# Kernel optimization log

Hardware: AMD Instinct MI355X
Metric: run time of the kernel (lower is better)

Reference implementation:

```python
import jax, jax.numpy as jnp
import numpy as np

N_NODES = 16384
N_EDGES = 196608
N_ELEM = 8
C = 32              # hidden channels per l-block
LMAX = 3
SH_DIM = 16         # (LMAX+1)^2
NUM_BESSEL = 8
R_MAX = 5.0
P_CUT = 5.0
H_RAD = 64
AVG_NEIGH = 12.0
N_LAYERS = 2
L_SLICES = ((0, 1), (1, 4), (4, 9), (9, 16))  # l = 0..3 blocks


def real_sph_harm(u):
    # u: [E,3] unit vectors -> real spherical harmonics up to l=3, component-normalized. [E,16]
    x, y, z = u[:, 0], u[:, 1], u[:, 2]
    x2, y2, z2 = x * x, y * y, z * z
    sh = [
        jnp.ones_like(x),
        jnp.sqrt(3.) * x, jnp.sqrt(3.) * y, jnp.sqrt(3.) * z,
        jnp.sqrt(15.) * x * y, jnp.sqrt(15.) * y * z,
        jnp.sqrt(5.) / 2. * (3. * z2 - 1.), jnp.sqrt(15.) * x * z,
        jnp.sqrt(15.) / 2. * (x2 - y2),
        jnp.sqrt(35. / 8.) * y * (3. * x2 - y2), jnp.sqrt(105.) * x * y * z,
        jnp.sqrt(21. / 8.) * y * (5. * z2 - 1.), jnp.sqrt(7.) / 2. * z * (5. * z2 - 3.),
        jnp.sqrt(21. / 8.) * x * (5. * z2 - 1.), jnp.sqrt(105.) / 2. * z * (x2 - y2),
        jnp.sqrt(35. / 8.) * x * (x2 - 3. * y2),
    ]
    return jnp.stack(sh, axis=-1)


def bessel_cutoff(r):
    # Bessel radial basis * polynomial cutoff (MACE radial embedding). r: [E] -> [E, NUM_BESSEL]
    u = r / R_MAX
    n = jnp.arange(1, NUM_BESSEL + 1, dtype=r.dtype)
    safe_r = jnp.maximum(r, 1e-9)
    rb = jnp.sqrt(2.0 / R_MAX) * jnp.sin(jnp.pi * n * u[:, None]) / safe_r[:, None]
    p = P_CUT
    fc = 1.0 - (p + 1.) * (p + 2.) / 2. * u ** p + p * (p + 2.) * u ** (p + 1.) - p * (p + 1.) / 2. * u ** (p + 2.)
    fc = fc * (u < 1.0).astype(r.dtype)
    return rb * fc[:, None]


def per_l_linear(a, W):
    # equivariant per-l channel mixing. a: [N,C,16], W: [4,C,C]
    outs = [jnp.einsum('nci,co->noi', a[:, :, s:e], W[l]) for l, (s, e) in enumerate(L_SLICES)]
    return jnp.concatenate(outs, axis=-1)


def mace_descriptors(atom_pos, node_attrs, shifts, edge_index,
                     W_embed, W1, W2, W3, W4, Wlin, Wskip, w2, w3, Wprod):
    snd, rcv = edge_index[0], edge_index[1]
    vec = atom_pos[rcv] - atom_pos[snd] + shifts            # [E,3]
    length = jnp.sqrt(jnp.sum(vec * vec, axis=-1) + 1e-18)  # [E]
    unit = vec / length[:, None]
    edge_attrs = real_sph_harm(unit)                        # [E,16]
    edge_feats = bessel_cutoff(length)                      # [E,8]

    node_scal = node_attrs @ W_embed                        # [N,C] node embedding (l=0)
    node_feats = jnp.zeros((atom_pos.shape[0], C, SH_DIM), dtype=atom_pos.dtype).at[:, :, 0].set(node_scal)

    descs = []
    for i in range(N_LAYERS):
        # radial MLP -> per-edge tensor-product weights
        h = jax.nn.silu(edge_feats @ W1[i])
        h = jax.nn.silu(h @ W2[i])
        h = jax.nn.silu(h @ W3[i])
        tpw = (h @ W4[i]).reshape(-1, C, SH_DIM)            # [E,C,16]
        # gather -> channelwise tensor product with edge spherical harmonics
        s = node_feats[:, :, 0][snd]                        # [E,C] invariant sender feats
        msg = tpw * edge_attrs[:, None, :] * s[:, :, None]  # [E,C,16]
        # scatter-add aggregation
        agg = jax.ops.segment_sum(msg.reshape(-1, C * SH_DIM), rcv,
                                  num_segments=N_NODES) / AVG_NEIGH
        a = per_l_linear(agg.reshape(-1, C, SH_DIM), Wlin[i])
        # element-dependent residual (skip tensor product with one-hot node attrs)
        sc = jnp.einsum('nz,ncm,zco->nom', node_attrs, node_feats, Wskip[i])
        # symmetric-contraction-style product block (correlation up to 3, invariants)
        inv = a[:, :, 0]
        p2 = jnp.sum(a * a, axis=-1)                        # power-spectrum invariant [N,C]
        b0 = inv + w2[i] * p2 + w3[i] * inv * p2
        b = a.at[:, :, 0].set(b0)
        node_feats = per_l_linear(b, Wprod[i]) + sc
        descs.append(node_feats[:, :, 0])                   # invariant slice
    return jnp.concatenate(descs, axis=-1)                  # [N, N_LAYERS*C]


def setup_inputs() -> dict:
    key = jax.random.key(0)
    ks = jax.random.split(key, 16)
    atom_pos = jax.random.normal(ks[0], (N_NODES, 3), dtype=jnp.float32) * 1.8
    elem = jax.random.randint(ks[1], (N_NODES,), 0, N_ELEM)
    node_attrs = jax.nn.one_hot(elem, N_ELEM, dtype=jnp.float32)
    shifts = jnp.zeros((N_EDGES, 3), dtype=jnp.float32)
    edge_index = jax.random.randint(ks[2], (2, N_EDGES), 0, N_NODES)
    f32 = jnp.float32
    W_embed = jax.random.normal(ks[3], (N_ELEM, C), f32) / np.sqrt(N_ELEM)
    W1 = jax.random.normal(ks[4], (N_LAYERS, NUM_BESSEL, H_RAD), f32) / np.sqrt(NUM_BESSEL)
    W2 = jax.random.normal(ks[5], (N_LAYERS, H_RAD, H_RAD), f32) / np.sqrt(H_RAD)
    W3 = jax.random.normal(ks[6], (N_LAYERS, H_RAD, H_RAD), f32) / np.sqrt(H_RAD)
    W4 = jax.random.normal(ks[7], (N_LAYERS, H_RAD, C * SH_DIM), f32) / np.sqrt(H_RAD)
    Wlin = jax.random.normal(ks[8], (N_LAYERS, 4, C, C), f32) / np.sqrt(C)
    Wskip = jax.random.normal(ks[9], (N_LAYERS, N_ELEM, C, C), f32) / np.sqrt(N_ELEM * C)
    w2 = jax.random.normal(ks[10], (N_LAYERS, C), f32) * 0.1
    w3 = jax.random.normal(ks[11], (N_LAYERS, C), f32) * 0.1
    Wprod = jax.random.normal(ks[12], (N_LAYERS, 4, C, C), f32) / np.sqrt(C)
    return {"atom_pos": atom_pos, "node_attrs": node_attrs, "shifts": shifts,
            "edge_index": edge_index, "W_embed": W_embed, "W1": W1, "W2": W2,
            "W3": W3, "W4": W4, "Wlin": Wlin, "Wskip": Wskip, "w2": w2,
            "w3": w3, "Wprod": Wprod}


def reference(atom_pos, node_attrs, shifts, edge_index, W_embed, W1, W2, W3, W4,
              Wlin, Wskip, w2, w3, Wprod):
    return mace_descriptors(atom_pos, node_attrs, shifts, edge_index,
                            W_embed, W1, W2, W3, W4, Wlin, Wskip, w2, w3, Wprod)
```

## Files before the change

### kernel.cpp

```cpp
#include <hip/hip_runtime.h>
#include <math.h>

#define N_NODES_C 16384
#define N_EDGES_C 196608
#define MAX_TILES 32768

typedef short bf16x8 __attribute__((ext_vector_type(8)));
typedef float f32x4 __attribute__((ext_vector_type(4)));
typedef float f32x8 __attribute__((ext_vector_type(8)));

__device__ __forceinline__ float silu_f(float x) {
  return x * __builtin_amdgcn_rcpf(1.0f + __expf(-x));
}

__global__ void k_count(const int* __restrict__ rcv, int* __restrict__ counts) {
  int e = blockIdx.x * 256 + threadIdx.x;
  atomicAdd(&counts[rcv[e]], 1);
}

__global__ __launch_bounds__(1024) void k_scan(const int* __restrict__ counts,
                                               int* __restrict__ row_start,
                                               int* __restrict__ cursor,
                                               int* __restrict__ tstart) {
  __shared__ int s1a[1024];
  __shared__ int s2a[1024];
  const int tid = threadIdx.x;
  int loc[16];
  int s1 = 0, s2 = 0;
#pragma unroll
  for (int i = 0; i < 16; ++i) {
    loc[i] = counts[tid * 16 + i];
    s1 += loc[i];
    s2 += (loc[i] + 15) >> 4;
  }
  s1a[tid] = s1;
  s2a[tid] = s2;
  __syncthreads();
  for (int off = 1; off < 1024; off <<= 1) {
    int t1 = (tid >= off) ? s1a[tid - off] : 0;
    int t2 = (tid >= off) ? s2a[tid - off] : 0;
    __syncthreads();
    s1a[tid] += t1;
    s2a[tid] += t2;
    __syncthreads();
  }
  int e1 = s1a[tid] - s1, e2 = s2a[tid] - s2;
#pragma unroll
  for (int i = 0; i < 16; ++i) {
    row_start[tid * 16 + i] = e1;
    cursor[tid * 16 + i] = e1;
    tstart[tid * 16 + i] = e2;
    e1 += loc[i];
    e2 += (loc[i] + 15) >> 4;
  }
  if (tid == 1023) {
    row_start[N_NODES_C] = e1;
    tstart[N_NODES_C] = e2;
  }
}

__global__ void k_fill(const int* __restrict__ rcv, int* __restrict__ cursor,
                       int* __restrict__ elist) {
  int e = blockIdx.x * 256 + threadIdx.x;
  int slot = atomicAdd(&cursor[rcv[e]], 1);
  elist[slot] = e;
}

__global__ void k_tiles(const int* __restrict__ row_start, const int* __restrict__ tstart,
                        int2* __restrict__ tdesc) {
  const int n = blockIdx.x * 256 + threadIdx.x;
  const int e0 = row_start[n], e1 = row_start[n + 1];
  const int cnt = e1 - e0;
  const int nt = (cnt + 15) >> 4;
  const int t0 = tstart[n];
  const unsigned mbit = (nt > 1) ? 0x80000000u : 0u;
  for (int j = 0; j < nt; ++j) {
    int len = cnt - 16 * j;
    if (len > 16) len = 16;
    tdesc[t0 + j] = make_int2((int)((unsigned)n | ((unsigned)len << 20) | mbit), e0 + 16 * j);
  }
}

__global__ void k_elem(const float* __restrict__ attrs, int* __restrict__ elem) {
  int n = blockIdx.x * 256 + threadIdx.x;
  const float* a = attrs + n * 8;
  int best = 0;
  float bv = a[0];
#pragma unroll
  for (int z = 1; z < 8; ++z) {
    if (a[z] > bv) { bv = a[z]; best = z; }
  }
  elem[n] = best;
}

__global__ void k_embed(const float* __restrict__ attrs, const float* __restrict__ Wemb,
                        float* __restrict__ scal0, float* __restrict__ nf) {
  int gid = blockIdx.x * 256 + threadIdx.x;
  int n = gid >> 5, c = gid & 31;
  float s = 0.f;
#pragma unroll
  for (int z = 0; z < 8; ++z) s = fmaf(attrs[n * 8 + z], Wemb[z * 32 + c], s);
  scal0[gid] = s;
  float* row = nf + (size_t)n * 512 + c * 16;
  *(float4*)&row[0] = make_float4(s, 0.f, 0.f, 0.f);
  *(float4*)&row[4] = make_float4(0.f, 0.f, 0.f, 0.f);
  *(float4*)&row[8] = make_float4(0.f, 0.f, 0.f, 0.f);
  *(float4*)&row[12] = make_float4(0.f, 0.f, 0.f, 0.f);
}

__global__ __launch_bounds__(256, 3) void k_radial(
    const float* __restrict__ pos, const float* __restrict__ shifts,
    const int* __restrict__ snd, const int* __restrict__ rcv,
    const int* __restrict__ elist, const float* __restrict__ scal,
    const float* __restrict__ W1g, const float* __restrict__ W2g,
    const float* __restrict__ W3g, unsigned short* __restrict__ h3,
    float* __restrict__ sedge, float* __restrict__ Yout, const int writeY) {
  __shared__ __align__(16) float efs[4][32][8];
  __shared__ __align__(16) float hbs[4][2][64];
  const int wid = threadIdx.x >> 6, lane = threadIdx.x & 63;
  float w1c[8], w2c[64], w3c[64];
#pragma unroll
  for (int k = 0; k < 8; ++k) w1c[k] = W1g[k * 64 + lane];
#pragma unroll
  for (int k = 0; k < 64; ++k) w2c[k] = W2g[k * 64 + lane];
#pragma unroll
  for (int k = 0; k < 64; ++k) w3c[k] = W3g[k * 64 + lane];

  const int base = (blockIdx.x * 4 + wid) * 32;

  if (lane < 32) {
    const int p = base + lane;
    const int e = elist[p];
    const int sn = snd[e], rc = rcv[e];
    const float vx = pos[rc * 3 + 0] - pos[sn * 3 + 0] + shifts[e * 3 + 0];
    const float vy = pos[rc * 3 + 1] - pos[sn * 3 + 1] + shifts[e * 3 + 1];
    const float vz = pos[rc * 3 + 2] - pos[sn * 3 + 2] + shifts[e * 3 + 2];
    const float len = __builtin_amdgcn_sqrtf(vx * vx + vy * vy + vz * vz + 1e-18f);
    const float u = len * 0.2f;
    float fc = 0.f;
    if (u < 1.0f) {
      const float u2 = u * u, u5 = u2 * u2 * u;
      fc = 1.0f - 21.0f * u5 + 35.0f * u5 * u - 15.0f * u5 * u2;
    }
    const float pref = 0.6324555320336759f * fc * __builtin_amdgcn_rcpf(fmaxf(len, 1e-9f));
    float efv[8];
#pragma unroll
    for (int k = 0; k < 8; ++k) {
      const float pin = 3.14159274f * (float)(k + 1);
      efv[k] = pref * __sinf(pin * u);
    }
    *(float4*)&efs[wid][lane][0] = make_float4(efv[0], efv[1], efv[2], efv[3]);
    *(float4*)&efs[wid][lane][4] = make_float4(efv[4], efv[5], efv[6], efv[7]);

    if (writeY) {
      const float il = __builtin_amdgcn_rcpf(len);
      const float x = vx * il, y = vy * il, z = vz * il;
      const float x2 = x * x, y2 = y * y, z2 = z * z;
      const float s3 = 1.7320508075688772f;
      const float s15 = 3.872983346207417f;
      const float s5h = 1.118033988749895f;
      const float s35_8 = 2.091650066335189f;
      const float s105 = 10.246950765959598f;
      const float s21_8 = 1.6201851746019651f;
      const float s7h = 1.3228756555322954f;
      const float s105h = 5.123475382979799f;
      float* yp = Yout + (size_t)p * 16;
      *(float4*)&yp[0] = make_float4(1.f, s3 * x, s3 * y, s3 * z);
      *(float4*)&yp[4] = make_float4(s15 * x * y, s15 * y * z, s5h * (3.f * z2 - 1.f), s15 * x * z);
      *(float4*)&yp[8] = make_float4(0.5f * s15 * (x2 - y2), s35_8 * y * (3.f * x2 - y2),
                                     s105 * x * y * z, s21_8 * y * (5.f * z2 - 1.f));
      *(float4*)&yp[12] = make_float4(s7h * z * (5.f * z2 - 3.f), s21_8 * x * (5.f * z2 - 1.f),
                                      s105h * z * (x2 - y2), s35_8 * x * (x2 - 3.f * y2));
    }
  }

  {
    const int p2 = base + (lane >> 1);
    const int e2 = elist[p2];
    const int sn2 = snd[e2];
    const int co = (lane & 1) * 16;
    const float* sp = scal + (size_t)sn2 * 32 + co;
    float* dp = sedge + (size_t)p2 * 32 + co;
    *(float4*)&dp[0] = *(const float4*)&sp[0];
    *(float4*)&dp[4] = *(const float4*)&sp[4];
    *(float4*)&dp[8] = *(const float4*)&sp[8];
    *(float4*)&dp[12] = *(const float4*)&sp[12];
  }

  for (int t = 0; t < 16; ++t) {
    const float4 eA0 = *(const float4*)&efs[wid][t][0];
    const float4 eA1 = *(const float4*)&efs[wid][t][4];
    const float4 eB0 = *(const float4*)&efs[wid][t + 16][0];
    const float4 eB1 = *(const float4*)&efs[wid][t + 16][4];
    float aA = eA0.x * w1c[0], aB = eB0.x * w1c[0];
    aA = fmaf(eA0.y, w1c[1], aA); aB = fmaf(eB0.y, w1c[1], aB);
    aA = fmaf(eA0.z, w1c[2], aA); aB = fmaf(eB0.z, w1c[2], aB);
    aA = fmaf(eA0.w, w1c[3], aA); aB = fmaf(eB0.w, w1c[3], aB);
    aA = fmaf(eA1.x, w1c[4], aA); aB = fmaf(eB1.x, w1c[4], aB);
    aA = fmaf(eA1.y, w1c[5], aA); aB = fmaf(eB1.y, w1c[5], aB);
    aA = fmaf(eA1.z, w1c[6], aA); aB = fmaf(eB1.z, w1c[6], aB);
    aA = fmaf(eA1.w, w1c[7], aA); aB = fmaf(eB1.w, w1c[7], aB);
    hbs[wid][0][lane] = silu_f(aA);
    hbs[wid][1][lane] = silu_f(aB);
    float pA0 = 0.f, pA1 = 0.f, pA2 = 0.f, pA3 = 0.f;
    float pB0 = 0.f, pB1 = 0.f, pB2 = 0.f, pB3 = 0.f;
#pragma unroll
    for (int k4 = 0; k4 < 16; ++k4) {
      const float4 hA = *(const float4*)&hbs[wid][0][k4 * 4];
      const float4 hB = *(const float4*)&hbs[wid][1][k4 * 4];
      pA0 = fmaf(hA.x, w2c[k4 * 4 + 0], pA0); pB0 = fmaf(hB.x, w2c[k4 * 4 + 0], pB0);
      pA1 = fmaf(hA.y, w2c[k4 * 4 + 1], pA1); pB1 = fmaf(hB.y, w2c[k4 * 4 + 1], pB1);
      pA2 = fmaf(hA.z, w2c[k4 * 4 + 2], pA2); pB2 = fmaf(hB.z, w2c[k4 * 4 + 2], pB2);
      pA3 = fmaf(hA.w, w2c[k4 * 4 + 3], pA3); pB3 = fmaf(hB.w, w2c[k4 * 4 + 3], pB3);
    }
    hbs[wid][0][lane] = silu_f((pA0 + pA1) + (pA2 + pA3));
    hbs[wid][1][lane] = silu_f((pB0 + pB1) + (pB2 + pB3));
    pA0 = pA1 = pA2 = pA3 = 0.f;
    pB0 = pB1 = pB2 = pB3 = 0.f;
#pragma unroll
    for (int k4 = 0; k4 < 16; ++k4) {
      const float4 hA = *(const float4*)&hbs[wid][0][k4 * 4];
      const float4 hB = *(const float4*)&hbs[wid][1][k4 * 4];
      pA0 = fmaf(hA.x, w3c[k4 * 4 + 0], pA0); pB0 = fmaf(hB.x, w3c[k4 * 4 + 0], pB0);
      pA1 = fmaf(hA.y, w3c[k4 * 4 + 1], pA1); pB1 = fmaf(hB.y, w3c[k4 * 4 + 1], pB1);
      pA2 = fmaf(hA.z, w3c[k4 * 4 + 2], pA2); pB2 = fmaf(hB.z, w3c[k4 * 4 + 2], pB2);
      pA3 = fmaf(hA.w, w3c[k4 * 4 + 3], pA3); pB3 = fmaf(hB.w, w3c[k4 * 4 + 3], pB3);
    }
    const float hvA = silu_f((pA0 + pA1) + (pA2 + pA3));
    const float hvB = silu_f((pB0 + pB1) + (pB2 + pB3));
    const unsigned hbA = __float_as_uint(hvA) & 0xFFFF0000u;
    const unsigned hbB = __float_as_uint(hvB) & 0xFFFF0000u;
    const float loA = hvA - __uint_as_float(hbA);
    const float loB = hvB - __uint_as_float(hbB);
    h3[(size_t)(base + t) * 128 + lane] = (unsigned short)(hbA >> 16);
    h3[(size_t)(base + t) * 128 + 64 + lane] = (unsigned short)(__float_as_uint(loA) >> 16);
    h3[(size_t)(base + 16 + t) * 128 + lane] = (unsigned short)(hbB >> 16);
    h3[(size_t)(base + 16 + t) * 128 + 64 + lane] = (unsigned short)(__float_as_uint(loB) >> 16);
  }
}

#define TLOAD(AX, YX, SX, MX, PX, tix)                                        \
  {                                                                           \
    const int tic = ((tix) < ntiles) ? (tix) : (ntiles - 1);                  \
    const int2 td = tdesc[tic];                                               \
    MX = (unsigned)td.x;                                                      \
    PX = td.y;                                                                \
    const unsigned short* hp = h3 + (size_t)(PX + lm) * 128 + grp * 8;        \
    AX##0 = *(const bf16x8*)(hp);                                             \
    AX##1 = *(const bf16x8*)(hp + 32);                                        \
    AX##2 = *(const bf16x8*)(hp + 64);                                        \
    AX##3 = *(const bf16x8*)(hp + 96);                                        \
    _Pragma("unroll") for (int r = 0; r < 4; ++r) {                           \
      const int pr = PX + grp * 4 + r;                                        \
      YX[r] = Yb[(size_t)pr * 16 + lm];                                       \
      SX[r] = *(const float4*)&sedge[(size_t)pr * 32 + cg * 4];               \
    }                                                                         \
  }

#define TCOMP(AX, YX, SX, MX, PX, tix)                                        \
  {                                                                           \
    const int node = (int)(MX & 0x3FFFu);                                     \
    const int len = (int)((MX >> 20) & 31u);                                  \
    const bool multi = (MX & 0x80000000u) != 0u;                              \
    float ys[4][4];                                                           \
    _Pragma("unroll") for (int r = 0; r < 4; ++r) {                           \
      const int rr = grp * 4 + r;                                             \
      const float Yv = (rr < len) ? YX[r] * inv12 : 0.f;                      \
      ys[r][0] = Yv * SX[r].x;                                                \
      ys[r][1] = Yv * SX[r].y;                                                \
      ys[r][2] = Yv * SX[r].z;                                                \
      ys[r][3] = Yv * SX[r].w;                                                \
    }                                                                         \
    float outv[4];                                                            \
    _Pragma("unroll") for (int t = 0; t < 4; ++t) {                           \
      f32x4 acc = {0.f, 0.f, 0.f, 0.f};                                       \
      acc = __builtin_amdgcn_mfma_f32_16x16x32_bf16(AX##0, bhi[t][0], acc, 0, 0, 0); \
      acc = __builtin_amdgcn_mfma_f32_16x16x32_bf16(AX##1, bhi[t][1], acc, 0, 0, 0); \
      acc = __builtin_amdgcn_mfma_f32_16x16x32_bf16(AX##2, bhi[t][0], acc, 0, 0, 0); \
      acc = __builtin_amdgcn_mfma_f32_16x16x32_bf16(AX##3, bhi[t][1], acc, 0, 0, 0); \
      acc = __builtin_amdgcn_mfma_f32_16x16x32_bf16(AX##0, blo[t][0], acc, 0, 0, 0); \
      acc = __builtin_amdgcn_mfma_f32_16x16x32_bf16(AX##1, blo[t][1], acc, 0, 0, 0); \
      float cp = acc[0] * ys[0][t];                                           \
      cp = fmaf(acc[1], ys[1][t], cp);                                        \
      cp = fmaf(acc[2], ys[2][t], cp);                                        \
      cp = fmaf(acc[3], ys[3][t], cp);                                        \
      cp += __shfl_xor(cp, 16);                                               \
      cp += __shfl_xor(cp, 32);                                               \
      outv[t] = cp;                                                           \
    }                                                                         \
    float sel = outv[0];                                                      \
    sel = (grp == 1) ? outv[1] : sel;                                         \
    sel = (grp == 2) ? outv[2] : sel;                                         \
    sel = (grp == 3) ? outv[3] : sel;                                         \
    if ((tix) < ntiles) {                                                     \
      float* ap = &agg[(size_t)node * 512 + cg * 64 + grp * 16 + lm];         \
      if (multi)                                                              \
        atomicAdd(ap, sel);                                                   \
      else                                                                    \
        *ap = sel;                                                            \
    }                                                                         \
  }

__global__ __launch_bounds__(256, 2) void k_gather(
    const unsigned short* __restrict__ h3, const float* __restrict__ W4g,
    const float* __restrict__ Yb, const float* __restrict__ sedge,
    const int2* __restrict__ tdesc, const int* __restrict__ ntiles_ptr,
    float* __restrict__ agg) {
  const int bid = blockIdx.x;
  const int xcd = bid & 7, q = bid >> 3, half = q & 1;
  const int s = ((q >> 1) << 3) | xcd;
  const int w = threadIdx.x >> 6, lane = threadIdx.x & 63;
  const int grp = lane >> 4, lm = lane & 15;
  const int cg = half * 4 + w;
  const float inv12 = 1.0f / 12.0f;

  bf16x8 bhi[4][2], blo[4][2];
#pragma unroll
  for (int t = 0; t < 4; ++t) {
    const int col = cg * 64 + t * 16 + lm;
#pragma unroll
    for (int kk = 0; kk < 2; ++kk) {
#pragma unroll
      for (int j = 0; j < 8; ++j) {
        const float wv = W4g[(kk * 32 + grp * 8 + j) * 512 + col];
        const unsigned hb = __float_as_uint(wv) & 0xFFFF0000u;
        bhi[t][kk][j] = (short)(hb >> 16);
        blo[t][kk][j] = (short)(__float_as_uint(wv - __uint_as_float(hb)) >> 16);
      }
    }
  }

  const int ntiles = *ntiles_ptr;
  const int chunk = (ntiles + 1023) >> 10;
  const int tbeg = s * chunk;

  bf16x8 aA0, aA1, aA2, aA3, aB0, aB1, aB2, aB3;
  float yA[4], yB[4];
  float4 sA[4], sB[4];
  unsigned mA, mB;
  int pA, pB;

  TLOAD(aA, yA, sA, mA, pA, tbeg);
  int j = 0;
  while (true) {
    TLOAD(aB, yB, sB, mB, pB, tbeg + j + 1);
    TCOMP(aA, yA, sA, mA, pA, tbeg + j);
    ++j;
    if (j >= chunk) break;
    TLOAD(aA, yA, sA, mA, pA, tbeg + j + 1);
    TCOMP(aB, yB, sB, mB, pB, tbeg + j);
    ++j;
    if (j >= chunk) break;
  }
}

__global__ __launch_bounds__(256) void k_node(
    const float* __restrict__ agg, float* __restrict__ nf,
    const float* __restrict__ Wlin, const float* __restrict__ Wprod,
    const float* __restrict__ Wskip, const float* __restrict__ w2v,
    const float* __restrict__ w3v, const int* __restrict__ elem,
    float* __restrict__ scal_out, float* __restrict__ dout, const int layer) {
  __shared__ __align__(16) float aggs[8][512];
  __shared__ __align__(16) float nfs[8][512];
  __shared__ float bs[8][544];
  const int tid = threadIdx.x;
  const int n0 = blockIdx.x * 8;
  for (int i = tid; i < 1024; i += 256) {
    const int nl = i >> 7, qq = i & 127;
    ((f32x4*)aggs)[i] = ((const f32x4*)agg)[(size_t)(n0 + nl) * 128 + qq];
    ((f32x4*)nfs)[i] = ((const f32x4*)nf)[(size_t)(n0 + nl) * 128 + qq];
  }
  __syncthreads();
  const int nl = tid >> 5, o = tid & 31;
  const int n = n0 + nl;
  constexpr int SLa[4] = {0, 1, 4, 9};
  constexpr int ELa[4] = {1, 4, 9, 16};
  float a[16];
#pragma unroll
  for (int m = 0; m < 16; ++m) a[m] = 0.f;
#pragma unroll
  for (int l = 0; l < 4; ++l) {
    for (int c = 0; c < 32; ++c) {
      const float w = Wlin[(l * 32 + c) * 32 + o];
#pragma unroll
      for (int m = SLa[l]; m < ELa[l]; ++m) a[m] = fmaf(aggs[nl][c * 16 + m], w, a[m]);
    }
  }
  const float inv = a[0];
  float p2 = 0.f;
#pragma unroll
  for (int m = 0; m < 16; ++m) p2 = fmaf(a[m], a[m], p2);
  a[0] = inv + w2v[o] * p2 + w3v[o] * inv * p2;
#pragma unroll
  for (int m = 0; m < 16; ++m) bs[nl][o * 17 + m] = a[m];
  __syncthreads();
  float outv[16];
#pragma unroll
  for (int m = 0; m < 16; ++m) outv[m] = 0.f;
#pragma unroll
  for (int l = 0; l < 4; ++l) {
    for (int c = 0; c < 32; ++c) {
      const float w = Wprod[(l * 32 + c) * 32 + o];
#pragma unroll
      for (int m = SLa[l]; m < ELa[l]; ++m) outv[m] = fmaf(bs[nl][c * 17 + m], w, outv[m]);
    }
  }
  const int z = elem[n];
  const float* wsk = Wskip + z * 1024;
  for (int c = 0; c < 32; ++c) {
    const float w = wsk[c * 32 + o];
#pragma unroll
    for (int m = 0; m < 16; ++m) outv[m] = fmaf(nfs[nl][c * 16 + m], w, outv[m]);
  }
  float* op = nf + (size_t)n * 512 + o * 16;
  *(float4*)&op[0] = make_float4(outv[0], outv[1], outv[2], outv[3]);
  *(float4*)&op[4] = make_float4(outv[4], outv[5], outv[6], outv[7]);
  *(float4*)&op[8] = make_float4(outv[8], outv[9], outv[10], outv[11]);
  *(float4*)&op[12] = make_float4(outv[12], outv[13], outv[14], outv[15]);
  scal_out[n * 32 + o] = outv[0];
  dout[(size_t)n * 64 + layer * 32 + o] = outv[0];
}

extern "C" void kernel_launch(void* const* d_in, const int* in_sizes, int n_in,
                              void* d_out, int out_size, void* d_ws, size_t ws_size,
                              hipStream_t stream) {
  const float* pos = (const float*)d_in[0];
  const float* attrs = (const float*)d_in[1];
  const float* shifts = (const float*)d_in[2];
  const int* eidx = (const int*)d_in[3];
  const float* W_embed = (const float*)d_in[4];
  const float* W1 = (const float*)d_in[5];
  const float* W2 = (const float*)d_in[6];
  const float* W3 = (const float*)d_in[7];
  const float* W4 = (const float*)d_in[8];
  const float* Wlin = (const float*)d_in[9];
  const float* Wskip = (const float*)d_in[10];
  const float* w2v = (const float*)d_in[11];
  const float* w3v = (const float*)d_in[12];
  const float* Wprod = (const float*)d_in[13];
  float* out = (float*)d_out;
  const int* snd = eidx;
  const int* rcv = eidx + N_EDGES_C;

  char* p = (char*)d_ws;
  auto take = [&](size_t bytes) {
    char* q = p;
    p += (bytes + 255) & ~(size_t)255;
    return q;
  };
  int* counts = (int*)take((size_t)N_NODES_C * 4);
  int* row_start = (int*)take((size_t)(N_NODES_C + 1) * 4);
  int* cursor = (int*)take((size_t)N_NODES_C * 4);
  int* tstart = (int*)take((size_t)(N_NODES_C + 1) * 4);
  int* elist = (int*)take((size_t)N_EDGES_C * 4);
  int2* tdesc = (int2*)take((size_t)MAX_TILES * 8);
  int* elem = (int*)take((size_t)N_NODES_C * 4);
  float* Ybuf = (float*)take((size_t)(N_EDGES_C + 16) * 16 * 4);
  unsigned short* h3 = (unsigned short*)take((size_t)(N_EDGES_C + 16) * 128 * 2);
  float* sedge = (float*)take((size_t)(N_EDGES_C + 16) * 32 * 4);
  float* agg = (float*)take((size_t)N_NODES_C * 512 * 4);
  float* nf = (float*)take((size_t)N_NODES_C * 512 * 4);
  float* scal0 = (float*)take((size_t)N_NODES_C * 32 * 4);
  float* scal1 = (float*)take((size_t)N_NODES_C * 32 * 4);
  (void)ws_size; (void)in_sizes; (void)n_in; (void)out_size;

  hipMemsetAsync(counts, 0, (size_t)N_NODES_C * 4, stream);
  k_count<<<N_EDGES_C / 256, 256, 0, stream>>>(rcv, counts);
  k_scan<<<1, 1024, 0, stream>>>(counts, row_start, cursor, tstart);
  k_fill<<<N_EDGES_C / 256, 256, 0, stream>>>(rcv, cursor, elist);
  k_tiles<<<N_NODES_C / 256, 256, 0, stream>>>(row_start, tstart, tdesc);
  k_elem<<<N_NODES_C / 256, 256, 0, stream>>>(attrs, elem);
  k_embed<<<N_NODES_C * 32 / 256, 256, 0, stream>>>(attrs, W_embed, scal0, nf);

  for (int i = 0; i < 2; ++i) {
    k_radial<<<1536, 256, 0, stream>>>(pos, shifts, snd, rcv, elist,
                                       i == 0 ? scal0 : scal1,
                                       W1 + (size_t)i * 8 * 64, W2 + (size_t)i * 64 * 64,
                                       W3 + (size_t)i * 64 * 64, h3, sedge, Ybuf,
                                       i == 0 ? 1 : 0);
    hipMemsetAsync(agg, 0, (size_t)N_NODES_C * 512 * 4, stream);
    k_gather<<<2048, 256, 0, stream>>>(h3, W4 + (size_t)i * 64 * 512, Ybuf, sedge,
                                       tdesc, tstart + N_NODES_C, agg);
    k_node<<<N_NODES_C / 8, 256, 0, stream>>>(agg, nf, Wlin + (size_t)i * 4096,
                                              Wprod + (size_t)i * 4096,
                                              Wskip + (size_t)i * 8192,
                                              w2v + (size_t)i * 32, w3v + (size_t)i * 32,
                                              elem, scal1, out, i);
  }
}
```

Measured before the change: 518.6 us.

## Deepen gather kernel prefetch to a four-slot ring and halve the grid

Replaces the two-stage double buffer in the edge-gather kernel with a four-slot ring. Tile descriptors are fetched four tiles ahead, and h3, Y and sedge data two tiles ahead, with the Y·sedge scaling done at load time. The grid drops from 2048 to 1024 blocks, so each block handles a chunk twice as long, rounded up to a multiple of four. The aim is to hide global-load latency behind the MFMA work. In exchange, register pressure rises, and the padded chunks add extra clamped tail iterations.

```diff
diff --git a/kernel.cpp b/kernel.cpp
--- a/kernel.cpp
+++ b/kernel.cpp
@@ -239,51 +239,56 @@
   }
 }
 
-#define TLOAD(AX, YX, SX, MX, PX, tix)                                        \
+#define MLOAD(K, tix)                                                         \
   {                                                                           \
     const int tic = ((tix) < ntiles) ? (tix) : (ntiles - 1);                  \
     const int2 td = tdesc[tic];                                               \
-    MX = (unsigned)td.x;                                                      \
-    PX = td.y;                                                                \
-    const unsigned short* hp = h3 + (size_t)(PX + lm) * 128 + grp * 8;        \
-    AX##0 = *(const bf16x8*)(hp);                                             \
-    AX##1 = *(const bf16x8*)(hp + 32);                                        \
-    AX##2 = *(const bf16x8*)(hp + 64);                                        \
-    AX##3 = *(const bf16x8*)(hp + 96);                                        \
-    _Pragma("unroll") for (int r = 0; r < 4; ++r) {                           \
-      const int pr = PX + grp * 4 + r;                                        \
-      YX[r] = Yb[(size_t)pr * 16 + lm];                                       \
-      SX[r] = *(const float4*)&sedge[(size_t)pr * 32 + cg * 4];               \
-    }                                                                         \
-  }
-
-#define TCOMP(AX, YX, SX, MX, PX, tix)                                        \
+    M[K] = (unsigned)td.x;                                                    \
+    P[K] = td.y;                                                              \
+  }
+
+#define DLOAD(K2)                                                             \
   {                                                                           \
-    const int node = (int)(MX & 0x3FFFu);                                     \
-    const int len = (int)((MX >> 20) & 31u);                                  \
-    const bool multi = (MX & 0x80000000u) != 0u;                              \
-    float ys[4][4];                                                           \
+    const int p0 = P[K2];                                                     \
+    const int lend = (int)((M[K2] >> 20) & 31u);                              \
+    const unsigned short* hp = h3 + (size_t)(p0 + lm) * 128 + grp * 8;        \
+    A[K2][0] = *(const bf16x8*)(hp);                                          \
+    A[K2][1] = *(const bf16x8*)(hp + 32);                                     \
+    A[K2][2] = *(const bf16x8*)(hp + 64);                                     \
+    A[K2][3] = *(const bf16x8*)(hp + 96);                                     \
     _Pragma("unroll") for (int r = 0; r < 4; ++r) {                           \
       const int rr = grp * 4 + r;                                             \
-      const float Yv = (rr < len) ? YX[r] * inv12 : 0.f;                      \
-      ys[r][0] = Yv * SX[r].x;                                                \
-      ys[r][1] = Yv * SX[r].y;                                                \
-      ys[r][2] = Yv * SX[r].z;                                                \
-      ys[r][3] = Yv * SX[r].w;                                                \
+      const int pr = p0 + rr;                                                 \
+      const float yr = Yb[(size_t)pr * 16 + lm];                              \
+      const float Yv = ((rr < lend) ? yr : 0.f) * inv12;                      \
+      const float4 s4 = *(const float4*)&sedge[(size_t)pr * 32 + cg * 4];     \
+      YS[K2][r][0] = Yv * s4.x;                                               \
+      YS[K2][r][1] = Yv * s4.y;                                               \
+      YS[K2][r][2] = Yv * s4.z;                                               \
+      YS[K2][r][3] = Yv * s4.w;                                               \
     }                                                                         \
+  }
+
+#define STEP(K)                                                               \
+  {                                                                           \
+    const unsigned mcur = M[K];                                               \
+    MLOAD(K, tb + 4);                                                         \
+    DLOAD((K + 2) & 3);                                                       \
+    const int node = (int)(mcur & 0x3FFFu);                                   \
+    const bool multi = (mcur & 0x80000000u) != 0u;                            \
     float outv[4];                                                            \
     _Pragma("unroll") for (int t = 0; t < 4; ++t) {                           \
       f32x4 acc = {0.f, 0.f, 0.f, 0.f};                                       \
-      acc = __builtin_amdgcn_mfma_f32_16x16x32_bf16(AX##0, bhi[t][0], acc, 0, 0, 0); \
-      acc = __builtin_amdgcn_mfma_f32_16x16x32_bf16(AX##1, bhi[t][1], acc, 0, 0, 0); \
-      acc = __builtin_amdgcn_mfma_f32_16x16x32_bf16(AX##2, bhi[t][0], acc, 0, 0, 0); \
-      acc = __builtin_amdgcn_mfma_f32_16x16x32_bf16(AX##3, bhi[t][1], acc, 0, 0, 0); \
-      acc = __builtin_amdgcn_mfma_f32_16x16x32_bf16(AX##0, blo[t][0], acc, 0, 0, 0); \
-      acc = __builtin_amdgcn_mfma_f32_16x16x32_bf16(AX##1, blo[t][1], acc, 0, 0, 0); \
-      float cp = acc[0] * ys[0][t];                                           \
-      cp = fmaf(acc[1], ys[1][t], cp);                                        \
-      cp = fmaf(acc[2], ys[2][t], cp);                                        \
-      cp = fmaf(acc[3], ys[3][t], cp);                                        \
+      acc = __builtin_amdgcn_mfma_f32_16x16x32_bf16(A[K][0], bhi[t][0], acc, 0, 0, 0); \
+      acc = __builtin_amdgcn_mfma_f32_16x16x32_bf16(A[K][1], bhi[t][1], acc, 0, 0, 0); \
+      acc = __builtin_amdgcn_mfma_f32_16x16x32_bf16(A[K][2], bhi[t][0], acc, 0, 0, 0); \
+      acc = __builtin_amdgcn_mfma_f32_16x16x32_bf16(A[K][3], bhi[t][1], acc, 0, 0, 0); \
+      acc = __builtin_amdgcn_mfma_f32_16x16x32_bf16(A[K][0], blo[t][0], acc, 0, 0, 0); \
+      acc = __builtin_amdgcn_mfma_f32_16x16x32_bf16(A[K][1], blo[t][1], acc, 0, 0, 0); \
+      float cp = acc[0] * YS[K][0][t];                                        \
+      cp = fmaf(acc[1], YS[K][1][t], cp);                                     \
+      cp = fmaf(acc[2], YS[K][2][t], cp);                                     \
+      cp = fmaf(acc[3], YS[K][3][t], cp);                                     \
       cp += __shfl_xor(cp, 16);                                               \
       cp += __shfl_xor(cp, 32);                                               \
       outv[t] = cp;                                                           \
@@ -292,13 +297,14 @@
     sel = (grp == 1) ? outv[1] : sel;                                         \
     sel = (grp == 2) ? outv[2] : sel;                                         \
     sel = (grp == 3) ? outv[3] : sel;                                         \
-    if ((tix) < ntiles) {                                                     \
+    if (tb < ntiles) {                                                        \
       float* ap = &agg[(size_t)node * 512 + cg * 64 + grp * 16 + lm];         \
       if (multi)                                                              \
         atomicAdd(ap, sel);                                                   \
       else                                                                    \
         *ap = sel;                                                            \
     }                                                                         \
+    ++tb;                                                                     \
   }
 
 __global__ __launch_bounds__(256, 2) void k_gather(
@@ -331,26 +337,26 @@
   }
 
   const int ntiles = *ntiles_ptr;
-  const int chunk = (ntiles + 1023) >> 10;
-  const int tbeg = s * chunk;
-
-  bf16x8 aA0, aA1, aA2, aA3, aB0, aB1, aB2, aB3;
-  float yA[4], yB[4];
-  float4 sA[4], sB[4];
-  unsigned mA, mB;
-  int pA, pB;
-
-  TLOAD(aA, yA, sA, mA, pA, tbeg);
-  int j = 0;
-  while (true) {
-    TLOAD(aB, yB, sB, mB, pB, tbeg + j + 1);
-    TCOMP(aA, yA, sA, mA, pA, tbeg + j);
-    ++j;
-    if (j >= chunk) break;
-    TLOAD(aA, yA, sA, mA, pA, tbeg + j + 1);
-    TCOMP(aB, yB, sB, mB, pB, tbeg + j);
-    ++j;
-    if (j >= chunk) break;
+  const int chunk4 = ((((ntiles + 511) >> 9) + 3) & ~3);
+  int tb = s * chunk4;
+
+  bf16x8 A[4][4];
+  float YS[4][4][4];
+  unsigned M[4];
+  int P[4];
+
+  MLOAD(0, tb + 0);
+  MLOAD(1, tb + 1);
+  MLOAD(2, tb + 2);
+  MLOAD(3, tb + 3);
+  DLOAD(0);
+  DLOAD(1);
+
+  for (int jj = 0; jj < chunk4; jj += 4) {
+    STEP(0);
+    STEP(1);
+    STEP(2);
+    STEP(3);
   }
 }
 
@@ -479,7 +485,7 @@
                                        W3 + (size_t)i * 64 * 64, h3, sedge, Ybuf,
                                        i == 0 ? 1 : 0);
     hipMemsetAsync(agg, 0, (size_t)N_NODES_C * 512 * 4, stream);
-    k_gather<<<2048, 256, 0, stream>>>(h3, W4 + (size_t)i * 64 * 512, Ybuf, sedge,
+    k_gather<<<1024, 256, 0, stream>>>(h3, W4 + (size_t)i * 64 * 512, Ybuf, sedge,
                                        tdesc, tstart + N_NODES_C, agg);
     k_node<<<N_NODES_C / 8, 256, 0, stream>>>(agg, nf, Wlin + (size_t)i * 4096,
                                               Wprod + (size_t)i * 4096,
```

After: 515.1 us. About the same (-0.7%).
